# Kernel tuning notes

Hardware: AMD Instinct MI355X
Metric: run time of the kernel (lower is better)

The kernel has to match this reference:

```python
import jax, jax.numpy as jnp
import numpy as np

# dims
B, T1, T2, SEG = 4, 16, 16, 4          # batch, src len, tgt len, max segment length
V, E, H, ENC = 8000, 256, 256, 512     # vocab, embed, lstm hidden, encoder units
EOS = 2                                 # end-of-segment symbol ($)
NEG = -1e30                             # finite -inf (grad-safe)


def setup_inputs():
    key = jax.random.key(0)
    ks = jax.random.split(key, 16)
    s = 0.05
    n = lambda k, shp: (jax.random.normal(k, shp) * s).astype(jnp.float32)
    return {
        "prev_output_tokens": jax.random.randint(ks[0], (B, T2), 0, V),
        "encoder_outs": jax.random.normal(ks[1], (T1, B, ENC), dtype=jnp.float32),
        "embed": n(ks[2], (V, E)),
        "start_embed": n(ks[3], (E,)),
        "proj_h_w": n(ks[4], (H, ENC)), "proj_h_b": jnp.zeros((H,), jnp.float32),
        "proj_c_w": n(ks[5], (H, ENC)), "proj_c_b": jnp.zeros((H,), jnp.float32),
        "w_ih0": n(ks[6], (4 * H, H + E)), "w_hh0": n(ks[7], (4 * H, H)), "b0": jnp.zeros((4 * H,), jnp.float32),
        "w_ih1": n(ks[8], (4 * H, H)), "w_hh1": n(ks[9], (4 * H, H)), "b1": jnp.zeros((4 * H,), jnp.float32),
        "fc_w": n(ks[10], (V, H)), "fc_b": jnp.zeros((V,), jnp.float32),
    }


def _lstm_cell(x, h, c, w_ih, w_hh, b):
    # PyTorch LSTMCell gate order: i, f, g, o
    g = x @ w_ih.T + h @ w_hh.T + b
    i, f, gg, o = jnp.split(g, 4, axis=-1)
    c_new = jax.nn.sigmoid(f) * c + jax.nn.sigmoid(i) * jnp.tanh(gg)
    h_new = jax.nn.sigmoid(o) * jnp.tanh(c_new)
    return h_new, c_new


def reference(prev_output_tokens, encoder_outs, embed, start_embed,
              proj_h_w, proj_h_b, proj_c_w, proj_c_b,
              w_ih0, w_hh0, b0, w_ih1, w_hh1, b1, fc_w, fc_b):
    y = prev_output_tokens                                     # [B, T2]
    # segment windows: tok[b, t2, k] = y[b, t2+k] (clipped; masked later via logpy mask)
    pos = jnp.arange(T2 + 1)[:, None] + jnp.arange(SEG)[None, :]   # [T2+1, SEG]
    tok = y[:, jnp.minimum(pos, T2 - 1)]                            # [B, T2+1, SEG]
    emb_tok = embed[tok]                                            # [B, T2+1, SEG, E]
    x0 = jnp.broadcast_to(start_embed, (B, T2 + 1, 1, E))
    xs = jnp.moveaxis(jnp.concatenate([x0, emb_tok], axis=2), 2, 0)  # [SEG+1, B, T2+1, E]
    tgt = jnp.concatenate([tok, jnp.zeros((B, T2 + 1, 1), tok.dtype)], axis=2)
    tgt = jnp.moveaxis(tgt, 2, 0)                                    # [SEG+1, B, T2+1]

    # per-encoder-position initial states / context (encoder proj, as in __init__)
    eo = jnp.swapaxes(encoder_outs, 0, 1)                            # [B, T1, ENC]
    h0 = eo @ proj_h_w.T + proj_h_b                                  # [B, T1, H]
    c0 = eo @ proj_c_w.T + proj_c_b
    ctx = jnp.broadcast_to(h0[:, :, None, :], (B, T1, T2 + 1, H))

    def step(carry, inp):
        h1, c1, h2, c2 = carry
        x, t = inp                                                   # x [B,T2+1,E], t [B,T2+1]
        xb = jnp.broadcast_to(x[:, None, :, :], (B, T1, T2 + 1, E))
        h1, c1 = _lstm_cell(jnp.concatenate([ctx, xb], axis=-1), h1, c1, w_ih0, w_hh0, b0)
        h2, c2 = _lstm_cell(h1, h2, c2, w_ih1, w_hh1, b1)
        logp = jax.nn.log_softmax(h2 @ fc_w.T + fc_b, axis=-1)       # [B,T1,T2+1,V]
        idx = jnp.broadcast_to(t[:, None, :, None], (B, T1, T2 + 1, 1))
        sel = jnp.take_along_axis(logp, idx, axis=-1)[..., 0]
        return (h1, c1, h2, c2), (sel, logp[..., EOS])

    carry0 = (ctx,
              jnp.broadcast_to(c0[:, :, None, :], (B, T1, T2 + 1, H)),
              jnp.zeros((B, T1, T2 + 1, H), jnp.float32),
              jnp.zeros((B, T1, T2 + 1, H), jnp.float32))
    _, (sel, eosp) = jax.lax.scan(step, carry0, (xs, tgt))           # each [SEG+1,B,T1,T2+1]

    # logpy[b,t1,t2,j] = sum_{k<j} logp_k(y[t2+k]) + logp_j(EOS)
    cum = jnp.concatenate([jnp.zeros((1, B, T1, T2 + 1), sel.dtype),
                           jnp.cumsum(sel[:SEG], axis=0)], axis=0)
    logpy = jnp.moveaxis(cum + eosp, 0, -1)                          # [B,T1,T2+1,SEG+1]
    jmask = (jnp.arange(T2 + 1)[:, None] + jnp.arange(SEG + 1)[None, :]) <= T2
    logpy = jnp.where(jmask[None, None], logpy, NEG)

    # semi-Markov forward DP: alpha[t1+1, t2] = LSE_j alpha[t1, t2-j] + logpy[t1, t2-j, j]
    alpha0 = jnp.full((B, T2 + 1), NEG, sel.dtype).at[:, 0].set(0.0)

    def dp(alpha, row):                                              # row [B, T2+1, SEG+1]
        v = alpha[:, :, None] + row
        shifted = jnp.stack(
            [jnp.pad(v[:, :T2 + 1 - j, j], ((0, 0), (j, 0)), constant_values=NEG)
             for j in range(SEG + 1)], axis=0)
        return jax.nn.logsumexp(shifted, axis=0), None

    alpha, _ = jax.lax.scan(dp, alpha0, jnp.moveaxis(logpy, 1, 0))
    return alpha[:, T2]                                              # log-likelihood per batch elem
```

## Files before the change

kernel.cpp:

```cpp
#include <hip/hip_runtime.h>
#include <math.h>

#define B 4
#define T1 16
#define T2 16
#define SEG 4
#define V 8000
#define E 256
#define H 256
#define ENC 512
#define EOS 2
#define NEGV -1e30f
#define G4 1024
#define NCELL 1088
#define T21 17
#define NL 272
#define MP 5504
#define NTM 43
#define NTN 63
#define NFCT (NTM*NTN)
#define NPART 126

typedef __attribute__((ext_vector_type(4))) float f32x4;
typedef __attribute__((ext_vector_type(8))) short bf16x8;

__device__ __forceinline__ float sigm(float x) { return 1.f / (1.f + __expf(-x)); }
__device__ __forceinline__ float ftanh(float x) { float e = __expf(2.f * x); return 1.f - 2.f / (e + 1.f); }
__device__ __forceinline__ float b2f(short x) {
    unsigned u = ((unsigned)(unsigned short)x) << 16;
    return __builtin_bit_cast(float, u);
}
__device__ __forceinline__ short f2b(float f) {
    unsigned u = __builtin_bit_cast(unsigned, f);
    unsigned r = (u + 0x7fffu + ((u >> 16) & 1u)) >> 16;
    return (short)r;
}

__device__ __forceinline__ int swz8(int row) { return (row & 7) ^ ((row & 3) << 1); }

__device__ __forceinline__ void stage64(const char* g0, size_t gstrideB, int kOffB, char* lds) {
    int tid = threadIdx.x;
#pragma unroll
    for (int it = 0; it < 8; ++it) {
        int chunk = it * 256 + tid;
        int row = chunk >> 5;
        int g = chunk & 31;
        const char* src = g0 + (size_t)row * gstrideB + kOffB + ((g ^ swz8(row)) << 4);
        __builtin_amdgcn_global_load_lds((const __attribute__((address_space(1))) void*)src,
                                         (__attribute__((address_space(3))) void*)(lds + chunk * 16),
                                         16, 0, 0);
    }
}
__device__ __forceinline__ bf16x8 lds_frag(const char* lds, int row, int col16) {
    return *(const bf16x8*)(lds + row * 512 + ((col16 ^ swz8(row)) << 4));
}
__device__ __forceinline__ void mma_tile(const char* smA, const char* smB,
                                         int wave, int ln, int kg, f32x4 acc[4]) {
#pragma unroll
    for (int ks = 0; ks < 8; ++ks) {
        bf16x8 a = lds_frag(smA, wave * 16 + ln, ks * 4 + kg);
#pragma unroll
        for (int nf = 0; nf < 4; ++nf) {
            bf16x8 b = lds_frag(smB, nf * 16 + ln, ks * 4 + kg);
            acc[nf] = __builtin_amdgcn_mfma_f32_16x16x32_bf16(a, b, acc[nf], 0, 0, 0);
        }
    }
}

__device__ __forceinline__ bf16x8 frag128(const char* lds, int row, int gl) {
    return *(const bf16x8*)(lds + row * 256 + ((gl ^ swz8(row)) << 4));
}

__global__ void k_setup(const float* __restrict__ fcw, const float* __restrict__ whh0,
                        const float* __restrict__ wih1, const float* __restrict__ whh1,
                        const float* __restrict__ phw, const float* __restrict__ pcw,
                        const float* __restrict__ wih0, const float* __restrict__ b1,
                        short* __restrict__ fcwbf, short* __restrict__ whh0i, short* __restrict__ w1i,
                        float* __restrict__ projhT, float* __restrict__ projcT,
                        float* __restrict__ ctxT, float* __restrict__ xT, float* __restrict__ b1i) {
    int bid = blockIdx.x, tid = threadIdx.x;
    if (bid < 2000) {
        int i = (bid * 256 + tid) * 4;
        float4 v = *(const float4*)&fcw[i];
        short4 o = { f2b(v.x), f2b(v.y), f2b(v.z), f2b(v.w) };
        *(short4*)&fcwbf[i] = o;
        return;
    }
    bid -= 2000;
    if (bid < 256) {
        int i = (bid * 256 + tid) * 4;
        int gp = i >> 8, k = i & 255;
        float4 v = *(const float4*)&whh0[(size_t)((gp & 3) * 256 + (gp >> 2)) * 256 + k];
        short4 o = { f2b(v.x), f2b(v.y), f2b(v.z), f2b(v.w) };
        *(short4*)&whh0i[i] = o;
        return;
    }
    bid -= 256;
    if (bid < 512) {
        int i = (bid * 256 + tid) * 4;
        int gp = i >> 9, k = i & 511;
        int g = (gp & 3) * 256 + (gp >> 2);
        const float* src = (k < 256) ? &wih1[(size_t)g * 256 + k] : &whh1[(size_t)g * 256 + (k - 256)];
        float4 v = *(const float4*)src;
        short4 o = { f2b(v.x), f2b(v.y), f2b(v.z), f2b(v.w) };
        *(short4*)&w1i[i] = o;
        return;
    }
    bid -= 512;
    if (bid < 128) {
        int i = (bid * 256 + tid) * 4;
        int k = i >> 8, r = i & 255;
        float4 o = { phw[(size_t)r * ENC + k], phw[(size_t)(r + 1) * ENC + k],
                     phw[(size_t)(r + 2) * ENC + k], phw[(size_t)(r + 3) * ENC + k] };
        *(float4*)&projhT[i] = o;
        return;
    }
    bid -= 128;
    if (bid < 128) {
        int i = (bid * 256 + tid) * 4;
        int k = i >> 8, r = i & 255;
        float4 o = { pcw[(size_t)r * ENC + k], pcw[(size_t)(r + 1) * ENC + k],
                     pcw[(size_t)(r + 2) * ENC + k], pcw[(size_t)(r + 3) * ENC + k] };
        *(float4*)&projcT[i] = o;
        return;
    }
    bid -= 128;
    if (bid < 512) {
        int i = (bid * 256 + tid) * 4;
        int g = i >> 9, k = i & 511;
        float4 v = *(const float4*)&wih0[i];
        float* base = (k < 256) ? &ctxT[(size_t)k * G4 + g] : &xT[(size_t)(k - 256) * G4 + g];
        base[0] = v.x; base[G4] = v.y; base[2 * G4] = v.z; base[3 * G4] = v.w;
        return;
    }
    bid -= 512;
    if (bid < 1) {
        float4 o = { b1[tid], b1[256 + tid], b1[512 + tid], b1[768 + tid] };
        *(float4*)&b1i[tid * 4] = o;
        return;
    }
}

__global__ void k_init_state(const float* __restrict__ enc, const float* __restrict__ phT,
                             const float* __restrict__ phb, const float* __restrict__ pcT,
                             const float* __restrict__ pcb, float* __restrict__ h0, float* __restrict__ c0) {
    __shared__ float eo[ENC];
    int bi = blockIdx.x;
    int b = bi / T1, i = bi % T1;
    int j = threadIdx.x;
    for (int e = j; e < ENC; e += 256) eo[e] = enc[(size_t)(i * B + b) * ENC + e];
    __syncthreads();
    float ha = phb[j], ca = pcb[j];
    for (int e = 0; e < ENC; ++e) {
        float x = eo[e];
        ha += x * phT[(size_t)e * H + j];
        ca += x * pcT[(size_t)e * H + j];
    }
    h0[(size_t)bi * H + j] = ha;
    c0[(size_t)bi * H + j] = ca;
}

__global__ void k_init2(const int* __restrict__ y, const float* __restrict__ embed, const float* __restrict__ se,
                        const float* __restrict__ h0, const float* __restrict__ c0,
                        const float* __restrict__ ctxT, const float* __restrict__ xT,
                        const float* __restrict__ b0,
                        float* __restrict__ c1, float* __restrict__ c2,
                        short* __restrict__ hcA, short* __restrict__ hcB,
                        float* __restrict__ pre_ctxi, float* __restrict__ pre_xi) {
    __shared__ float sb[256];
    int bid = blockIdx.x, j = threadIdx.x;
    if (bid < NCELL) {
        int cell = bid, bi = cell / T21;
        c1[(size_t)cell * H + j] = c0[(size_t)bi * H + j];
        c2[(size_t)cell * H + j] = 0.f;
        hcA[(size_t)cell * 512 + j] = f2b(h0[(size_t)bi * H + j]);
        hcB[(size_t)cell * 512 + 256 + j] = 0;
        return;
    }
    bid -= NCELL;
    if (bid < 64) {
        int bi = bid;
        sb[j] = h0[(size_t)bi * H + j];
        __syncthreads();
        float a0 = b0[j], a1 = b0[256 + j], a2 = b0[512 + j], a3 = b0[768 + j];
        for (int k = 0; k < H; ++k) {
            float x = sb[k];
            const float* w = ctxT + (size_t)k * G4;
            a0 += x * w[j]; a1 += x * w[256 + j]; a2 += x * w[512 + j]; a3 += x * w[768 + j];
        }
        *(float4*)&pre_ctxi[(size_t)bi * G4 + 4 * j] = make_float4(a0, a1, a2, a3);
        return;
    }
    bid -= 64;
    int row = bid;
    int s = row / (B * T21), rem = row % (B * T21);
    int b = rem / T21, t = rem % T21;
    const float* src;
    if (s == 0) src = se;
    else { int tt = t + s - 1; if (tt > 15) tt = 15; src = embed + (size_t)y[b * T2 + tt] * E; }
    sb[j] = src[j];
    __syncthreads();
    float a0 = 0, a1 = 0, a2 = 0, a3 = 0;
    for (int k = 0; k < E; ++k) {
        float x = sb[k];
        const float* w = xT + (size_t)k * G4;
        a0 += x * w[j]; a1 += x * w[256 + j]; a2 += x * w[512 + j]; a3 += x * w[768 + j];
    }
    *(float4*)&pre_xi[(size_t)row * G4 + 4 * j] = make_float4(a0, a1, a2, a3);
}

__device__ __forceinline__ void lstm0_body(int step, int l, char* smA, char* smB,
        const short* __restrict__ IN, const short* __restrict__ whh0i,
        const float* __restrict__ pre_ctxi, const float* __restrict__ pre_xi,
        float* __restrict__ c1, short* __restrict__ OUT) {
    int tid = threadIdx.x;
    int wave = tid >> 6, lane = tid & 63, ln = lane & 15, kg = lane >> 4;
    int mb = l >> 4, nb = l & 15;
    int m0 = mb * 64, n0 = nb * 64;
    stage64((const char*)(IN + (size_t)m0 * 512), 1024, 0, smA);
    stage64((const char*)(whh0i + (size_t)n0 * 256), 512, 0, smB);
    __syncthreads();
    f32x4 acc[4] = {};
    mma_tile(smA, smB, wave, ln, kg, acc);
    __syncthreads();
    float* sg = (float*)smA;
#pragma unroll
    for (int nf = 0; nf < 4; ++nf)
#pragma unroll
        for (int r = 0; r < 4; ++r)
            sg[(wave * 16 + kg * 4 + r) * 68 + nf * 16 + ln] = acc[nf][r];
    __syncthreads();
    int jlo = nb * 16;
#pragma unroll
    for (int q2 = 0; q2 < 4; ++q2) {
        int item = q2 * 256 + tid;
        int c = item >> 4, jj = item & 15;
        int cell = m0 + c;
        int j = jlo + jj;
        float4 g = *(float4*)&sg[c * 68 + 4 * jj];
        int bi = cell / T21;
        int bb = bi >> 4;
        int t = cell % T21;
        int prow = (step * B + bb) * T21 + t;
        float4 pc = *(const float4*)&pre_ctxi[(size_t)bi * G4 + 4 * j];
        float4 px = *(const float4*)&pre_xi[(size_t)prow * G4 + 4 * j];
        float ig = g.x + pc.x + px.x, fg = g.y + pc.y + px.y;
        float gg = g.z + pc.z + px.z, og = g.w + pc.w + px.w;
        float cold = c1[(size_t)cell * H + j];
        float cn = sigm(fg) * cold + sigm(ig) * ftanh(gg);
        float hn = sigm(og) * ftanh(cn);
        c1[(size_t)cell * H + j] = cn;
        OUT[(size_t)cell * 512 + j] = f2b(hn);
    }
}

__device__ __forceinline__ void lstm1_body(int l, char* smA, char* smB,
        const short* __restrict__ IN, const short* __restrict__ w1i,
        const float* __restrict__ b1i, float* __restrict__ c2,
        short* __restrict__ slab, short* __restrict__ OUT) {
    int tid = threadIdx.x;
    int wave = tid >> 6, lane = tid & 63, ln = lane & 15, kg = lane >> 4;
    int mb = l >> 4, nb = l & 15;
    int m0 = mb * 64, n0 = nb * 64;
    f32x4 acc[4] = {};
#pragma unroll
    for (int kh = 0; kh < 2; ++kh) {
        if (kh) __syncthreads();
        stage64((const char*)(IN + (size_t)m0 * 512), 1024, kh * 512, smA);
        stage64((const char*)(w1i + (size_t)n0 * 512), 1024, kh * 512, smB);
        __syncthreads();
        mma_tile(smA, smB, wave, ln, kg, acc);
    }
    __syncthreads();
    float* sg = (float*)smA;
#pragma unroll
    for (int nf = 0; nf < 4; ++nf)
#pragma unroll
        for (int r = 0; r < 4; ++r)
            sg[(wave * 16 + kg * 4 + r) * 68 + nf * 16 + ln] = acc[nf][r];
    __syncthreads();
    int jlo = nb * 16;
#pragma unroll
    for (int q2 = 0; q2 < 4; ++q2) {
        int item = q2 * 256 + tid;
        int c = item >> 4, jj = item & 15;
        int cell = m0 + c;
        int j = jlo + jj;
        float4 g = *(float4*)&sg[c * 68 + 4 * jj];
        float4 bv = *(const float4*)&b1i[4 * j];
        float ig = g.x + bv.x, fg = g.y + bv.y, gg = g.z + bv.z, og = g.w + bv.w;
        float cold = c2[(size_t)cell * H + j];
        float cn = sigm(fg) * cold + sigm(ig) * ftanh(gg);
        float hn = sigm(og) * ftanh(cn);
        c2[(size_t)cell * H + j] = cn;
        short hb = f2b(hn);
        slab[(size_t)cell * 256 + j] = hb;
        OUT[(size_t)cell * 512 + 256 + j] = hb;
    }
}

__global__ __launch_bounds__(256, 2) void k_lstm(int s, int n_l1,
        const short* __restrict__ IN, short* __restrict__ OUT, short* __restrict__ slab,
        const short* __restrict__ whh0i, const short* __restrict__ w1i,
        const float* __restrict__ pre_ctxi, const float* __restrict__ pre_xi,
        const float* __restrict__ b1i, float* __restrict__ c1, float* __restrict__ c2) {
    __shared__ char smem[65536];
    char* smA = smem;
    char* smB = smem + 32768;
    int bx = blockIdx.x;
    if (bx < n_l1) lstm1_body(bx, smA, smB, IN, w1i, b1i, c2, slab, OUT);
    else lstm0_body(s + 1, bx - n_l1, smA, smB, IN, whh0i, pre_ctxi, pre_xi, c1, OUT);
}

__global__ __launch_bounds__(256, 2) void k_fc(const short* __restrict__ h2base, const short* __restrict__ Wv,
        const float* __restrict__ fcb, float* __restrict__ psum) {
    __shared__ char smem[65536];
    char* smA = smem;
    char* smB = smem + 32768;
    int bx = blockIdx.x;
    int xcd = bx & 7, idx = bx >> 3;
    int q = NFCT >> 3, r = NFCT & 7;
    int tl = xcd * q + (xcd < r ? xcd : r) + idx;
    int nb = tl / NTM, mb = tl % NTM;
    int m0 = mb * 128, n0 = nb * 128;
    int tid = threadIdx.x;
    int wave = tid >> 6, lane = tid & 63, ln = lane & 15, kg = lane >> 4;
    int wm = wave >> 1, wn = wave & 1;
    f32x4 acc[4][4] = {};
#pragma unroll
    for (int kh = 0; kh < 2; ++kh) {
        if (kh) __syncthreads();
#pragma unroll
        for (int it = 0; it < 8; ++it) {
            int chunk = it * 256 + tid;
            int row = chunk >> 4;
            int g = chunk & 15;
            const char* src = (const char*)(h2base + (size_t)(m0 + row) * 256)
                              + kh * 256 + ((g ^ swz8(row)) << 4);
            __builtin_amdgcn_global_load_lds((const __attribute__((address_space(1))) void*)src,
                                             (__attribute__((address_space(3))) void*)(smA + chunk * 16),
                                             16, 0, 0);
        }
#pragma unroll
        for (int it = 0; it < 8; ++it) {
            int chunk = it * 256 + tid;
            int row = chunk >> 4;
            int g = chunk & 15;
            int grow = n0 + row; if (grow > V - 1) grow = V - 1;
            const char* src = (const char*)(Wv + (size_t)grow * 256)
                              + kh * 256 + ((g ^ swz8(row)) << 4);
            __builtin_amdgcn_global_load_lds((const __attribute__((address_space(1))) void*)src,
                                             (__attribute__((address_space(3))) void*)(smB + chunk * 16),
                                             16, 0, 0);
        }
        __syncthreads();
#pragma unroll
        for (int ks = 0; ks < 4; ++ks) {
            bf16x8 a[4], b[4];
#pragma unroll
            for (int mf = 0; mf < 4; ++mf) a[mf] = frag128(smA, wm * 64 + mf * 16 + ln, ks * 4 + kg);
#pragma unroll
            for (int nf = 0; nf < 4; ++nf) b[nf] = frag128(smB, wn * 64 + nf * 16 + ln, ks * 4 + kg);
#pragma unroll
            for (int mf = 0; mf < 4; ++mf)
#pragma unroll
                for (int nf = 0; nf < 4; ++nf)
                    acc[mf][nf] = __builtin_amdgcn_mfma_f32_16x16x32_bf16(a[mf], b[nf], acc[mf][nf], 0, 0, 0);
        }
    }
    float rs[4][4];
#pragma unroll
    for (int mf = 0; mf < 4; ++mf)
#pragma unroll
        for (int r2 = 0; r2 < 4; ++r2) rs[mf][r2] = 0.f;
#pragma unroll
    for (int nf = 0; nf < 4; ++nf) {
        int col = n0 + wn * 64 + nf * 16 + ln;
        float fbn = (col < V) ? fcb[col] : NEGV;
#pragma unroll
        for (int mf = 0; mf < 4; ++mf)
#pragma unroll
            for (int r2 = 0; r2 < 4; ++r2)
                rs[mf][r2] += __expf(acc[mf][nf][r2] + fbn);
    }
#pragma unroll
    for (int mask = 1; mask < 16; mask <<= 1)
#pragma unroll
        for (int mf = 0; mf < 4; ++mf)
#pragma unroll
            for (int r2 = 0; r2 < 4; ++r2)
                rs[mf][r2] += __shfl_xor(rs[mf][r2], mask);
    if (ln == 0) {
#pragma unroll
        for (int mf = 0; mf < 4; ++mf)
#pragma unroll
            for (int r2 = 0; r2 < 4; ++r2)
                psum[(size_t)(nb * 2 + wn) * MP + m0 + wm * 64 + mf * 16 + kg * 4 + r2] = rs[mf][r2];
    }
}

__global__ void k_combine(const short* __restrict__ h2all, const short* __restrict__ Wv,
        const float* __restrict__ fcb, const int* __restrict__ y,
        const float* __restrict__ psum, float* __restrict__ sel, float* __restrict__ eosp) {
    int cb = blockIdx.x;
    int s = cb / 17, blk = cb % 17;
    int tid = threadIdx.x;
    int cl = tid >> 2, q = tid & 3;
    int cell = blk * 64 + cl;
    int b = cell / (T1 * T21);
    int t = cell % T21;
    int tv = 0;
    if (s < SEG) { int tt = t + s; if (tt > 15) tt = 15; tv = y[b * T2 + tt]; }
    const short* hp = h2all + (size_t)(s + 1) * NCELL * 256 + (size_t)cell * 256 + q * 64;
    const short* w1 = Wv + (size_t)tv * 256 + q * 64;
    const short* w2 = Wv + (size_t)EOS * 256 + q * 64;
    float d1 = 0.f, d2 = 0.f;
#pragma unroll
    for (int u = 0; u < 8; ++u) {
        bf16x8 av  = *(const bf16x8*)(hp + u * 8);
        bf16x8 wv1 = *(const bf16x8*)(w1 + u * 8);
        bf16x8 wv2 = *(const bf16x8*)(w2 + u * 8);
#pragma unroll
        for (int e = 0; e < 8; ++e) {
            float a = b2f(av[e]);
            d1 += a * b2f(wv1[e]);
            d2 += a * b2f(wv2[e]);
        }
    }
    d1 += __shfl_xor(d1, 1); d1 += __shfl_xor(d1, 2);
    d2 += __shfl_xor(d2, 1); d2 += __shfl_xor(d2, 2);
    int col = s * NCELL + cell;
    float ss = 0.f;
    for (int v2 = q * 32; v2 < q * 32 + 32 && v2 < NPART; ++v2)
        ss += psum[(size_t)v2 * MP + col];
    ss += __shfl_xor(ss, 1); ss += __shfl_xor(ss, 2);
    if (q == 0) {
        float lse = __logf(ss);
        sel[s * NCELL + cell]  = d1 + fcb[tv]  - lse;
        eosp[s * NCELL + cell] = d2 + fcb[EOS] - lse;
    }
}

__global__ void k_dp(const float* __restrict__ sel, const float* __restrict__ eosp, float* __restrict__ out) {
    __shared__ float row[SEG + 1][NCELL];
    __shared__ float alpha[B][T21];
    int tid = threadIdx.x;
    for (int c = tid; c < NCELL; c += 256) {
        float cum = 0.f;
        row[0][c] = eosp[c];
#pragma unroll
        for (int j = 1; j <= SEG; ++j) {
            cum += sel[(j - 1) * NCELL + c];
            row[j][c] = cum + eosp[j * NCELL + c];
        }
    }
    int b = tid / T21, t = tid % T21;
    bool act = tid < B * T21;
    if (act) alpha[b][t] = (t == 0) ? 0.f : NEGV;
    __syncthreads();
    for (int i = 0; i < T1; ++i) {
        float val = NEGV;
        if (act) {
            float terms[SEG + 1];
            float mx = -3.4e38f;
            int cnt2 = 0;
            for (int j = 0; j <= SEG && j <= t; ++j) {
                int cell = (b * T1 + i) * T21 + (t - j);
                float term = alpha[b][t - j] + row[j][cell];
                terms[cnt2++] = term;
                mx = fmaxf(mx, term);
            }
            float ssum = 0.f;
            for (int k2 = 0; k2 < cnt2; ++k2) ssum += __expf(terms[k2] - mx);
            val = mx + __logf(ssum);
        }
        __syncthreads();
        if (act) alpha[b][t] = val;
        __syncthreads();
    }
    if (act && t == T2) out[b] = alpha[b][T2];
}

extern "C" void kernel_launch(void* const* d_in, const int* in_sizes, int n_in,
                              void* d_out, int out_size, void* d_ws, size_t ws_size,
                              hipStream_t stream) {
    const int*   y     = (const int*)d_in[0];
    const float* enc   = (const float*)d_in[1];
    const float* embed = (const float*)d_in[2];
    const float* se    = (const float*)d_in[3];
    const float* phw   = (const float*)d_in[4];
    const float* phb   = (const float*)d_in[5];
    const float* pcw   = (const float*)d_in[6];
    const float* pcb   = (const float*)d_in[7];
    const float* wih0  = (const float*)d_in[8];
    const float* whh0  = (const float*)d_in[9];
    const float* b0    = (const float*)d_in[10];
    const float* wih1  = (const float*)d_in[11];
    const float* whh1  = (const float*)d_in[12];
    const float* b1    = (const float*)d_in[13];
    const float* fcw   = (const float*)d_in[14];
    const float* fcb   = (const float*)d_in[15];

    float* ws = (float*)d_ws;
    size_t off = 0;
    auto alloc = [&](size_t n) { float* p = ws + off; off += n; return p; };
    float* projhT   = alloc((size_t)ENC * H);
    float* projcT   = alloc((size_t)ENC * H);
    float* ctxT     = alloc((size_t)H * G4);
    float* xT       = alloc((size_t)E * G4);
    float* h0       = alloc((size_t)B * T1 * H);
    float* c0       = alloc((size_t)B * T1 * H);
    float* pre_ctxi = alloc((size_t)B * T1 * G4);
    float* pre_xi   = alloc((size_t)(SEG + 1) * B * T21 * G4);
    float* c1       = alloc((size_t)NCELL * H);
    float* c2       = alloc((size_t)NCELL * H);
    float* b1i      = alloc((size_t)G4);
    float* selbuf   = alloc((size_t)(SEG + 1) * NCELL);
    float* eospbuf  = alloc((size_t)(SEG + 1) * NCELL);
    float* psum     = alloc((size_t)NPART * MP);
    short* hc0      = (short*)alloc((size_t)NCELL * 512 / 2);
    short* hc1      = (short*)alloc((size_t)NCELL * 512 / 2);
    short* h2all    = (short*)alloc(((size_t)6 * NCELL + 64) * 256 / 2);
    short* whh0i    = (short*)alloc((size_t)G4 * 256 / 2);
    short* w1i      = (short*)alloc((size_t)G4 * 512 / 2);
    short* fcwbf    = (short*)alloc((size_t)V * H / 2);

    hipLaunchKernelGGL(k_setup, dim3(3537), dim3(256), 0, stream,
                       fcw, whh0, wih1, whh1, phw, pcw, wih0, b1,
                       fcwbf, whh0i, w1i, projhT, projcT, ctxT, xT, b1i);
    hipLaunchKernelGGL(k_init_state, dim3(B * T1), dim3(256), 0, stream,
                       enc, projhT, phb, projcT, pcb, h0, c0);
    hipLaunchKernelGGL(k_init2, dim3(NCELL + 64 + (SEG + 1) * B * T21), dim3(256), 0, stream,
                       y, embed, se, h0, c0, ctxT, xT, b0, c1, c2, hc0, hc1,
                       pre_ctxi, pre_xi);

    short* hcb[2] = { hc0, hc1 };
    hipLaunchKernelGGL(k_lstm, dim3(NL), dim3(256), 0, stream,
                       -1, 0, hcb[0], hcb[1], h2all,
                       whh0i, w1i, pre_ctxi, pre_xi, b1i, c1, c2);
    for (int s = 0; s < SEG; ++s) {
        hipLaunchKernelGGL(k_lstm, dim3(2 * NL), dim3(256), 0, stream,
                           s, NL, hcb[(s + 1) & 1], hcb[s & 1],
                           h2all + (size_t)(s + 1) * NCELL * 256,
                           whh0i, w1i, pre_ctxi, pre_xi, b1i, c1, c2);
    }
    hipLaunchKernelGGL(k_lstm, dim3(NL), dim3(256), 0, stream,
                       4, NL, hcb[1], hcb[0],
                       h2all + (size_t)5 * NCELL * 256,
                       whh0i, w1i, pre_ctxi, pre_xi, b1i, c1, c2);

    hipLaunchKernelGGL(k_fc, dim3(NFCT), dim3(256), 0, stream,
                       h2all + (size_t)NCELL * 256, fcwbf, fcb, psum);
    hipLaunchKernelGGL(k_combine, dim3(85), dim3(256), 0, stream,
                       h2all, fcwbf, fcb, y, psum, selbuf, eospbuf);
    hipLaunchKernelGGL(k_dp, dim3(1), dim3(256), 0, stream, selbuf, eospbuf, (float*)d_out);
}
```

Baseline: 186.6 us.

## Fuse all phases into one cooperative persistent kernel with grid syncs

Replaces the chain of roughly a dozen separate kernel launches (setup, init, per-step LSTM, FC, combine, DP) with a single cooperative kernel of 256 blocks that runs each phase in grid-stride loops separated by grid-wide barriers. This removes per-launch overhead and the gaps between dependent launches. In exchange each phase is limited to a fixed grid of 256 blocks with a 128KB LDS footprint, which lowers occupancy for the wide phases such as the FC GEMM and setup. Grid syncs also cost time. If the cooperative launch fails, it falls back to per-phase launches.

```diff
diff --git a/kernel.cpp b/kernel.cpp
--- a/kernel.cpp
+++ b/kernel.cpp
@@ -1,5 +1,8 @@
 #include <hip/hip_runtime.h>
+#include <hip/hip_cooperative_groups.h>
 #include <math.h>
+
+namespace cg = cooperative_groups;
 
 #define B 4
 #define T1 16
@@ -14,15 +17,25 @@
 #define G4 1024
 #define NCELL 1088
 #define T21 17
-#define NL 272
 #define MP 5504
 #define NTM 43
-#define NTN 63
-#define NFCT (NTM*NTN)
 #define NPART 126
+#define GRID 256
 
 typedef __attribute__((ext_vector_type(4))) float f32x4;
 typedef __attribute__((ext_vector_type(8))) short bf16x8;
+
+struct P {
+    const int* y; const float* enc; const float* embed; const float* se;
+    const float* phw; const float* phb; const float* pcw; const float* pcb;
+    const float* wih0; const float* whh0; const float* b0;
+    const float* wih1; const float* whh1; const float* b1;
+    const float* fcw; const float* fcb;
+    float *projhT, *projcT, *ctxT, *xT, *h0, *c0, *pre_ctxi, *pre_xi, *c1, *c2, *b1i;
+    float *selbuf, *eospbuf, *psum;
+    short *hc0, *hc1, *h2all, *whh0i, *w1i, *fcwbf;
+    float* out;
+};
 
 __device__ __forceinline__ float sigm(float x) { return 1.f / (1.f + __expf(-x)); }
 __device__ __forceinline__ float ftanh(float x) { float e = __expf(2.f * x); return 1.f - 2.f / (e + 1.f); }
@@ -35,7 +48,6 @@
     unsigned r = (u + 0x7fffu + ((u >> 16) & 1u)) >> 16;
     return (short)r;
 }
-
 __device__ __forceinline__ int swz8(int row) { return (row & 7) ^ ((row & 3) << 1); }
 
 __device__ __forceinline__ void stage64(const char* g0, size_t gstrideB, int kOffB, char* lds) {
@@ -66,164 +78,145 @@
         }
     }
 }
-
 __device__ __forceinline__ bf16x8 frag128(const char* lds, int row, int gl) {
     return *(const bf16x8*)(lds + row * 256 + ((gl ^ swz8(row)) << 4));
 }
 
-__global__ void k_setup(const float* __restrict__ fcw, const float* __restrict__ whh0,
-                        const float* __restrict__ wih1, const float* __restrict__ whh1,
-                        const float* __restrict__ phw, const float* __restrict__ pcw,
-                        const float* __restrict__ wih0, const float* __restrict__ b1,
-                        short* __restrict__ fcwbf, short* __restrict__ whh0i, short* __restrict__ w1i,
-                        float* __restrict__ projhT, float* __restrict__ projcT,
-                        float* __restrict__ ctxT, float* __restrict__ xT, float* __restrict__ b1i) {
-    int bid = blockIdx.x, tid = threadIdx.x;
-    if (bid < 2000) {
-        int i = (bid * 256 + tid) * 4;
-        float4 v = *(const float4*)&fcw[i];
-        short4 o = { f2b(v.x), f2b(v.y), f2b(v.z), f2b(v.w) };
-        *(short4*)&fcwbf[i] = o;
-        return;
-    }
-    bid -= 2000;
-    if (bid < 256) {
-        int i = (bid * 256 + tid) * 4;
-        int gp = i >> 8, k = i & 255;
-        float4 v = *(const float4*)&whh0[(size_t)((gp & 3) * 256 + (gp >> 2)) * 256 + k];
-        short4 o = { f2b(v.x), f2b(v.y), f2b(v.z), f2b(v.w) };
-        *(short4*)&whh0i[i] = o;
-        return;
-    }
-    bid -= 256;
-    if (bid < 512) {
-        int i = (bid * 256 + tid) * 4;
-        int gp = i >> 9, k = i & 511;
-        int g = (gp & 3) * 256 + (gp >> 2);
-        const float* src = (k < 256) ? &wih1[(size_t)g * 256 + k] : &whh1[(size_t)g * 256 + (k - 256)];
-        float4 v = *(const float4*)src;
-        short4 o = { f2b(v.x), f2b(v.y), f2b(v.z), f2b(v.w) };
-        *(short4*)&w1i[i] = o;
-        return;
-    }
-    bid -= 512;
-    if (bid < 128) {
-        int i = (bid * 256 + tid) * 4;
-        int k = i >> 8, r = i & 255;
-        float4 o = { phw[(size_t)r * ENC + k], phw[(size_t)(r + 1) * ENC + k],
-                     phw[(size_t)(r + 2) * ENC + k], phw[(size_t)(r + 3) * ENC + k] };
-        *(float4*)&projhT[i] = o;
-        return;
-    }
-    bid -= 128;
-    if (bid < 128) {
-        int i = (bid * 256 + tid) * 4;
-        int k = i >> 8, r = i & 255;
-        float4 o = { pcw[(size_t)r * ENC + k], pcw[(size_t)(r + 1) * ENC + k],
-                     pcw[(size_t)(r + 2) * ENC + k], pcw[(size_t)(r + 3) * ENC + k] };
-        *(float4*)&projcT[i] = o;
-        return;
-    }
-    bid -= 128;
-    if (bid < 512) {
-        int i = (bid * 256 + tid) * 4;
-        int g = i >> 9, k = i & 511;
-        float4 v = *(const float4*)&wih0[i];
-        float* base = (k < 256) ? &ctxT[(size_t)k * G4 + g] : &xT[(size_t)(k - 256) * G4 + g];
-        base[0] = v.x; base[G4] = v.y; base[2 * G4] = v.z; base[3 * G4] = v.w;
-        return;
-    }
-    bid -= 512;
-    if (bid < 1) {
-        float4 o = { b1[tid], b1[256 + tid], b1[512 + tid], b1[768 + tid] };
-        *(float4*)&b1i[tid * 4] = o;
-        return;
-    }
-}
-
-__global__ void k_init_state(const float* __restrict__ enc, const float* __restrict__ phT,
-                             const float* __restrict__ phb, const float* __restrict__ pcT,
-                             const float* __restrict__ pcb, float* __restrict__ h0, float* __restrict__ c0) {
-    __shared__ float eo[ENC];
+
+__device__ void phase_setup(const P& p) {
+    int tid = threadIdx.x;
+    for (int u = blockIdx.x; u < 3537; u += gridDim.x) {
+        int bid = u;
+        if (bid < 2000) {
+            int i = (bid * 256 + tid) * 4;
+            float4 v = *(const float4*)&p.fcw[i];
+            short4 o = { f2b(v.x), f2b(v.y), f2b(v.z), f2b(v.w) };
+            *(short4*)&p.fcwbf[i] = o;
+            continue;
+        }
+        bid -= 2000;
+        if (bid < 256) {
+            int i = (bid * 256 + tid) * 4;
+            int gp = i >> 8, k = i & 255;
+            float4 v = *(const float4*)&p.whh0[(size_t)((gp & 3) * 256 + (gp >> 2)) * 256 + k];
+            short4 o = { f2b(v.x), f2b(v.y), f2b(v.z), f2b(v.w) };
+            *(short4*)&p.whh0i[i] = o;
+            continue;
+        }
+        bid -= 256;
+        if (bid < 512) {
+            int i = (bid * 256 + tid) * 4;
+            int gp = i >> 9, k = i & 511;
+            int g = (gp & 3) * 256 + (gp >> 2);
+            const float* src = (k < 256) ? &p.wih1[(size_t)g * 256 + k] : &p.whh1[(size_t)g * 256 + (k - 256)];
+            float4 v = *(const float4*)src;
+            short4 o = { f2b(v.x), f2b(v.y), f2b(v.z), f2b(v.w) };
+            *(short4*)&p.w1i[i] = o;
+            continue;
+        }
+        bid -= 512;
+        if (bid < 128) {
+            int i = (bid * 256 + tid) * 4;
+            int k = i >> 8, r = i & 255;
+            float4 o = { p.phw[(size_t)r * ENC + k], p.phw[(size_t)(r + 1) * ENC + k],
+                         p.phw[(size_t)(r + 2) * ENC + k], p.phw[(size_t)(r + 3) * ENC + k] };
+            *(float4*)&p.projhT[i] = o;
+            continue;
+        }
+        bid -= 128;
+        if (bid < 128) {
+            int i = (bid * 256 + tid) * 4;
+            int k = i >> 8, r = i & 255;
+            float4 o = { p.pcw[(size_t)r * ENC + k], p.pcw[(size_t)(r + 1) * ENC + k],
+                         p.pcw[(size_t)(r + 2) * ENC + k], p.pcw[(size_t)(r + 3) * ENC + k] };
+            *(float4*)&p.projcT[i] = o;
+            continue;
+        }
+        bid -= 128;
+        if (bid < 512) {
+            int i = (bid * 256 + tid) * 4;
+            int g = i >> 9, k = i & 511;
+            float4 v = *(const float4*)&p.wih0[i];
+            float* base = (k < 256) ? &p.ctxT[(size_t)k * G4 + g] : &p.xT[(size_t)(k - 256) * G4 + g];
+            base[0] = v.x; base[G4] = v.y; base[2 * G4] = v.z; base[3 * G4] = v.w;
+            continue;
+        }
+        bid -= 512;
+        if (bid < 1) {
+            float4 o = { p.b1[tid], p.b1[256 + tid], p.b1[512 + tid], p.b1[768 + tid] };
+            *(float4*)&p.b1i[tid * 4] = o;
+        }
+    }
+}
+
+__device__ void phase_init_state(const P& p, char* smem) {
     int bi = blockIdx.x;
+    if (bi >= 64) return;
+    float* eo = (float*)smem;
     int b = bi / T1, i = bi % T1;
     int j = threadIdx.x;
-    for (int e = j; e < ENC; e += 256) eo[e] = enc[(size_t)(i * B + b) * ENC + e];
-    __syncthreads();
-    float ha = phb[j], ca = pcb[j];
+    for (int e = j; e < ENC; e += 256) eo[e] = p.enc[(size_t)(i * B + b) * ENC + e];
+    __syncthreads();
+    float ha = p.phb[j], ca = p.pcb[j];
     for (int e = 0; e < ENC; ++e) {
         float x = eo[e];
-        ha += x * phT[(size_t)e * H + j];
-        ca += x * pcT[(size_t)e * H + j];
-    }
-    h0[(size_t)bi * H + j] = ha;
-    c0[(size_t)bi * H + j] = ca;
-}
-
-__global__ void k_init2(const int* __restrict__ y, const float* __restrict__ embed, const float* __restrict__ se,
-                        const float* __restrict__ h0, const float* __restrict__ c0,
-                        const float* __restrict__ ctxT, const float* __restrict__ xT,
-                        const float* __restrict__ b0,
-                        float* __restrict__ c1, float* __restrict__ c2,
-                        short* __restrict__ hcA, short* __restrict__ hcB,
-                        float* __restrict__ pre_ctxi, float* __restrict__ pre_xi) {
-    __shared__ float sb[256];
-    int bid = blockIdx.x, j = threadIdx.x;
-    if (bid < NCELL) {
-        int cell = bid, bi = cell / T21;
-        c1[(size_t)cell * H + j] = c0[(size_t)bi * H + j];
-        c2[(size_t)cell * H + j] = 0.f;
-        hcA[(size_t)cell * 512 + j] = f2b(h0[(size_t)bi * H + j]);
-        hcB[(size_t)cell * 512 + 256 + j] = 0;
-        return;
-    }
-    bid -= NCELL;
-    if (bid < 64) {
-        int bi = bid;
-        sb[j] = h0[(size_t)bi * H + j];
-        __syncthreads();
-        float a0 = b0[j], a1 = b0[256 + j], a2 = b0[512 + j], a3 = b0[768 + j];
-        for (int k = 0; k < H; ++k) {
+        ha += x * p.projhT[(size_t)e * H + j];
+        ca += x * p.projcT[(size_t)e * H + j];
+    }
+    p.h0[(size_t)bi * H + j] = ha;
+    p.c0[(size_t)bi * H + j] = ca;
+}
+
+__device__ void phase_init2(const P& p, char* smem) {
+    float* sb = (float*)smem;
+    int j = threadIdx.x;
+    for (int u = blockIdx.x; u < NCELL + 64 + (SEG + 1) * B * T21; u += gridDim.x) {
+        int bid = u;
+        if (bid < NCELL) {
+            int cell = bid, bi = cell / T21;
+            p.c1[(size_t)cell * H + j] = p.c0[(size_t)bi * H + j];
+            p.c2[(size_t)cell * H + j] = 0.f;
+            p.hc0[(size_t)cell * 512 + j] = f2b(p.h0[(size_t)bi * H + j]);
+            p.hc1[(size_t)cell * 512 + 256 + j] = 0;
+            continue;
+        }
+        bid -= NCELL;
+        if (bid < 64) {
+            int bi = bid;
+            __syncthreads();
+            sb[j] = p.h0[(size_t)bi * H + j];
+            __syncthreads();
+            float a0 = p.b0[j], a1 = p.b0[256 + j], a2 = p.b0[512 + j], a3 = p.b0[768 + j];
+            for (int k = 0; k < H; ++k) {
+                float x = sb[k];
+                const float* w = p.ctxT + (size_t)k * G4;
+                a0 += x * w[j]; a1 += x * w[256 + j]; a2 += x * w[512 + j]; a3 += x * w[768 + j];
+            }
+            *(float4*)&p.pre_ctxi[(size_t)bi * G4 + 4 * j] = make_float4(a0, a1, a2, a3);
+            continue;
+        }
+        bid -= 64;
+        int row = bid;
+        int s = row / (B * T21), rem = row % (B * T21);
+        int b = rem / T21, t = rem % T21;
+        const float* src;
+        if (s == 0) src = p.se;
+        else { int tt = t + s - 1; if (tt > 15) tt = 15; src = p.embed + (size_t)p.y[b * T2 + tt] * E; }
+        __syncthreads();
+        sb[j] = src[j];
+        __syncthreads();
+        float a0 = 0, a1 = 0, a2 = 0, a3 = 0;
+        for (int k = 0; k < E; ++k) {
             float x = sb[k];
-            const float* w = ctxT + (size_t)k * G4;
+            const float* w = p.xT + (size_t)k * G4;
             a0 += x * w[j]; a1 += x * w[256 + j]; a2 += x * w[512 + j]; a3 += x * w[768 + j];
         }
-        *(float4*)&pre_ctxi[(size_t)bi * G4 + 4 * j] = make_float4(a0, a1, a2, a3);
-        return;
-    }
-    bid -= 64;
-    int row = bid;
-    int s = row / (B * T21), rem = row % (B * T21);
-    int b = rem / T21, t = rem % T21;
-    const float* src;
-    if (s == 0) src = se;
-    else { int tt = t + s - 1; if (tt > 15) tt = 15; src = embed + (size_t)y[b * T2 + tt] * E; }
-    sb[j] = src[j];
-    __syncthreads();
-    float a0 = 0, a1 = 0, a2 = 0, a3 = 0;
-    for (int k = 0; k < E; ++k) {
-        float x = sb[k];
-        const float* w = xT + (size_t)k * G4;
-        a0 += x * w[j]; a1 += x * w[256 + j]; a2 += x * w[512 + j]; a3 += x * w[768 + j];
-    }
-    *(float4*)&pre_xi[(size_t)row * G4 + 4 * j] = make_float4(a0, a1, a2, a3);
-}
-
-__device__ __forceinline__ void lstm0_body(int step, int l, char* smA, char* smB,
-        const short* __restrict__ IN, const short* __restrict__ whh0i,
-        const float* __restrict__ pre_ctxi, const float* __restrict__ pre_xi,
-        float* __restrict__ c1, short* __restrict__ OUT) {
-    int tid = threadIdx.x;
-    int wave = tid >> 6, lane = tid & 63, ln = lane & 15, kg = lane >> 4;
-    int mb = l >> 4, nb = l & 15;
-    int m0 = mb * 64, n0 = nb * 64;
-    stage64((const char*)(IN + (size_t)m0 * 512), 1024, 0, smA);
-    stage64((const char*)(whh0i + (size_t)n0 * 256), 512, 0, smB);
-    __syncthreads();
-    f32x4 acc[4] = {};
-    mma_tile(smA, smB, wave, ln, kg, acc);
-    __syncthreads();
-    float* sg = (float*)smA;
+        *(float4*)&p.pre_xi[(size_t)row * G4 + 4 * j] = make_float4(a0, a1, a2, a3);
+    }
+}
+
+__device__ void epi_l0(const P& p, float* sg, f32x4 acc[4], int m0, int nb, int step, short* OUT) {
+    int tid = threadIdx.x, wave = tid >> 6, lane = tid & 63, ln = lane & 15, kg = lane >> 4;
 #pragma unroll
     for (int nf = 0; nf < 4; ++nf)
 #pragma unroll
@@ -242,43 +235,28 @@
         int bb = bi >> 4;
         int t = cell % T21;
         int prow = (step * B + bb) * T21 + t;
-        float4 pc = *(const float4*)&pre_ctxi[(size_t)bi * G4 + 4 * j];
-        float4 px = *(const float4*)&pre_xi[(size_t)prow * G4 + 4 * j];
+        float4 pc = *(const float4*)&p.pre_ctxi[(size_t)bi * G4 + 4 * j];
+        float4 px = *(const float4*)&p.pre_xi[(size_t)prow * G4 + 4 * j];
         float ig = g.x + pc.x + px.x, fg = g.y + pc.y + px.y;
         float gg = g.z + pc.z + px.z, og = g.w + pc.w + px.w;
-        float cold = c1[(size_t)cell * H + j];
+        float cold = p.c1[(size_t)cell * H + j];
         float cn = sigm(fg) * cold + sigm(ig) * ftanh(gg);
         float hn = sigm(og) * ftanh(cn);
-        c1[(size_t)cell * H + j] = cn;
+        p.c1[(size_t)cell * H + j] = cn;
         OUT[(size_t)cell * 512 + j] = f2b(hn);
     }
-}
-
-__device__ __forceinline__ void lstm1_body(int l, char* smA, char* smB,
-        const short* __restrict__ IN, const short* __restrict__ w1i,
-        const float* __restrict__ b1i, float* __restrict__ c2,
-        short* __restrict__ slab, short* __restrict__ OUT) {
-    int tid = threadIdx.x;
-    int wave = tid >> 6, lane = tid & 63, ln = lane & 15, kg = lane >> 4;
-    int mb = l >> 4, nb = l & 15;
-    int m0 = mb * 64, n0 = nb * 64;
-    f32x4 acc[4] = {};
-#pragma unroll
-    for (int kh = 0; kh < 2; ++kh) {
-        if (kh) __syncthreads();
-        stage64((const char*)(IN + (size_t)m0 * 512), 1024, kh * 512, smA);
-        stage64((const char*)(w1i + (size_t)n0 * 512), 1024, kh * 512, smB);
-        __syncthreads();
-        mma_tile(smA, smB, wave, ln, kg, acc);
-    }
-    __syncthreads();
-    float* sg = (float*)smA;
+    __syncthreads();
+}
+
+__device__ void epi_l1(const P& p, float* sg, f32x4 acc[4], int m0, int nb, int s, short* OUT, bool writeOUT) {
+    int tid = threadIdx.x, wave = tid >> 6, lane = tid & 63, ln = lane & 15, kg = lane >> 4;
 #pragma unroll
     for (int nf = 0; nf < 4; ++nf)
 #pragma unroll
         for (int r = 0; r < 4; ++r)
             sg[(wave * 16 + kg * 4 + r) * 68 + nf * 16 + ln] = acc[nf][r];
     __syncthreads();
+    short* slab = p.h2all + (size_t)(s + 1) * NCELL * 256;
     int jlo = nb * 16;
 #pragma unroll
     for (int q2 = 0; q2 < 4; ++q2) {
@@ -287,122 +265,181 @@
         int cell = m0 + c;
         int j = jlo + jj;
         float4 g = *(float4*)&sg[c * 68 + 4 * jj];
-        float4 bv = *(const float4*)&b1i[4 * j];
+        float4 bv = *(const float4*)&p.b1i[4 * j];
         float ig = g.x + bv.x, fg = g.y + bv.y, gg = g.z + bv.z, og = g.w + bv.w;
-        float cold = c2[(size_t)cell * H + j];
+        float cold = p.c2[(size_t)cell * H + j];
         float cn = sigm(fg) * cold + sigm(ig) * ftanh(gg);
         float hn = sigm(og) * ftanh(cn);
-        c2[(size_t)cell * H + j] = cn;
+        p.c2[(size_t)cell * H + j] = cn;
         short hb = f2b(hn);
         slab[(size_t)cell * 256 + j] = hb;
-        OUT[(size_t)cell * 512 + 256 + j] = hb;
-    }
-}
-
-__global__ __launch_bounds__(256, 2) void k_lstm(int s, int n_l1,
-        const short* __restrict__ IN, short* __restrict__ OUT, short* __restrict__ slab,
-        const short* __restrict__ whh0i, const short* __restrict__ w1i,
-        const float* __restrict__ pre_ctxi, const float* __restrict__ pre_xi,
-        const float* __restrict__ b1i, float* __restrict__ c1, float* __restrict__ c2) {
-    __shared__ char smem[65536];
-    char* smA = smem;
-    char* smB = smem + 32768;
-    int bx = blockIdx.x;
-    if (bx < n_l1) lstm1_body(bx, smA, smB, IN, w1i, b1i, c2, slab, OUT);
-    else lstm0_body(s + 1, bx - n_l1, smA, smB, IN, whh0i, pre_ctxi, pre_xi, c1, OUT);
-}
-
-__global__ __launch_bounds__(256, 2) void k_fc(const short* __restrict__ h2base, const short* __restrict__ Wv,
-        const float* __restrict__ fcb, float* __restrict__ psum) {
-    __shared__ char smem[65536];
-    char* smA = smem;
-    char* smB = smem + 32768;
-    int bx = blockIdx.x;
-    int xcd = bx & 7, idx = bx >> 3;
-    int q = NFCT >> 3, r = NFCT & 7;
-    int tl = xcd * q + (xcd < r ? xcd : r) + idx;
-    int nb = tl / NTM, mb = tl % NTM;
-    int m0 = mb * 128, n0 = nb * 128;
-    int tid = threadIdx.x;
+        if (writeOUT) OUT[(size_t)cell * 512 + 256 + j] = hb;
+    }
+    __syncthreads();
+}
+
+__device__ void phase_lstm(const P& p, char* smem, int s1, int s0, bool doB) {
+    int bx = blockIdx.x, tid = threadIdx.x;
     int wave = tid >> 6, lane = tid & 63, ln = lane & 15, kg = lane >> 4;
-    int wm = wave >> 1, wn = wave & 1;
-    f32x4 acc[4][4] = {};
+    int nb = bx & 15, mb = bx >> 4;
+    char* A  = smem;
+    char* B0 = smem + 32768;
+    char* B1 = smem + 65536;
+    char* B2 = smem + 98304;
+    if (doB) {
+        stage64((const char*)(p.whh0i + (size_t)nb * 64 * 256), 512, 0, B0);
+        stage64((const char*)(p.w1i + (size_t)nb * 64 * 512), 1024, 0, B1);
+        stage64((const char*)(p.w1i + (size_t)nb * 64 * 512), 1024, 512, B2);
+    }
+    int sin = (s0 >= 0) ? s0 - 1 : s1;
+    const short* IN = ((sin + 1) & 1) ? p.hc1 : p.hc0;
+    short* OUT = (sin & 1) ? p.hc1 : p.hc0;
+    f32x4 acc1[4] = {}, acc0[4] = {};
+    stage64((const char*)(IN + (size_t)mb * 64 * 512), 1024, 0, A);
+    __syncthreads();
+    if (s1 >= 0) mma_tile(A, B1, wave, ln, kg, acc1);
+    if (s0 >= 0) mma_tile(A, B0, wave, ln, kg, acc0);
+    __syncthreads();
+    if (s1 >= 0) {
+        stage64((const char*)(IN + (size_t)mb * 64 * 512), 1024, 512, A);
+        __syncthreads();
+        mma_tile(A, B2, wave, ln, kg, acc1);
+        __syncthreads();
+        epi_l1(p, (float*)A, acc1, mb * 64, nb, s1, OUT, s1 != SEG);
+    }
+    if (s0 >= 0)
+        epi_l0(p, (float*)A, acc0, mb * 64, nb, s0, OUT);
+    if (s1 >= 0 && mb == 15) {
+        f32x4 e1[4] = {};
+        stage64((const char*)(IN + (size_t)1024 * 512), 1024, 0, A);
+        __syncthreads();
+        mma_tile(A, B1, wave, ln, kg, e1);
+        __syncthreads();
+        stage64((const char*)(IN + (size_t)1024 * 512), 1024, 512, A);
+        __syncthreads();
+        mma_tile(A, B2, wave, ln, kg, e1);
+        __syncthreads();
+        epi_l1(p, (float*)A, e1, 1024, nb, s1, OUT, s1 != SEG);
+    }
+    if (s0 >= 0 && mb == 14) {
+        f32x4 e0[4] = {};
+        stage64((const char*)(IN + (size_t)1024 * 512), 1024, 0, A);
+        __syncthreads();
+        mma_tile(A, B0, wave, ln, kg, e0);
+        __syncthreads();
+        epi_l0(p, (float*)A, e0, 1024, nb, s0, OUT);
+    }
+}
+
+__device__ void phase_fc(const P& p, char* smem) {
+    int bx = blockIdx.x, tid = threadIdx.x;
+    char* Ab0 = smem;
+    char* Ab1 = smem + 32768;
+    char* Bh0 = smem + 65536;
+    char* Bh1 = smem + 98304;
+    int t6 = bx & 63, w2 = bx >> 6;
+    int nb, w;
+    if (t6 == 63) { nb = w2; w = 4; } else { nb = t6; w = w2; }
+    int nw = (nb < 4) ? 5 : 4;
+    int n0 = nb * 128;
 #pragma unroll
     for (int kh = 0; kh < 2; ++kh) {
-        if (kh) __syncthreads();
-#pragma unroll
-        for (int it = 0; it < 8; ++it) {
-            int chunk = it * 256 + tid;
-            int row = chunk >> 4;
-            int g = chunk & 15;
-            const char* src = (const char*)(h2base + (size_t)(m0 + row) * 256)
-                              + kh * 256 + ((g ^ swz8(row)) << 4);
-            __builtin_amdgcn_global_load_lds((const __attribute__((address_space(1))) void*)src,
-                                             (__attribute__((address_space(3))) void*)(smA + chunk * 16),
-                                             16, 0, 0);
-        }
+        char* dst = kh ? Bh1 : Bh0;
 #pragma unroll
         for (int it = 0; it < 8; ++it) {
             int chunk = it * 256 + tid;
             int row = chunk >> 4;
             int g = chunk & 15;
             int grow = n0 + row; if (grow > V - 1) grow = V - 1;
-            const char* src = (const char*)(Wv + (size_t)grow * 256)
-                              + kh * 256 + ((g ^ swz8(row)) << 4);
+            const char* src = (const char*)(p.fcwbf + (size_t)grow * 256) + kh * 256 + ((g ^ swz8(row)) << 4);
             __builtin_amdgcn_global_load_lds((const __attribute__((address_space(1))) void*)src,
-                                             (__attribute__((address_space(3))) void*)(smB + chunk * 16),
+                                             (__attribute__((address_space(3))) void*)(dst + chunk * 16),
                                              16, 0, 0);
         }
-        __syncthreads();
+    }
+    int mbs[11]; int cnt = 0;
+    for (int mb = w; mb < NTM; mb += nw) mbs[cnt++] = mb;
+    const short* h2base = p.h2all + (size_t)NCELL * 256;
+    auto stageA = [&](int mb, int kh, char* buf) {
+#pragma unroll
+        for (int it = 0; it < 8; ++it) {
+            int chunk = it * 256 + tid;
+            int row = chunk >> 4;
+            int g = chunk & 15;
+            const char* src = (const char*)(h2base + (size_t)(mb * 128 + row) * 256) + kh * 256 + ((g ^ swz8(row)) << 4);
+            __builtin_amdgcn_global_load_lds((const __attribute__((address_space(1))) void*)src,
+                                             (__attribute__((address_space(3))) void*)(buf + chunk * 16),
+                                             16, 0, 0);
+        }
+    };
+    stageA(mbs[0], 0, Ab0);
+    __syncthreads();
+    int wave = tid >> 6, lane = tid & 63, ln = lane & 15, kg = lane >> 4;
+    int wm = wave >> 1, wn = wave & 1;
+    f32x4 acc[4][4] = {};
+    int nst = cnt * 2;
+    for (int st = 0; st < nst; ++st) {
+        int mb = mbs[st >> 1], kh = st & 1;
+        if (st + 1 < nst) stageA(mbs[(st + 1) >> 1], (st + 1) & 1, ((st + 1) & 1) ? Ab1 : Ab0);
+        char* Acur = (st & 1) ? Ab1 : Ab0;
+        char* Bcur = kh ? Bh1 : Bh0;
 #pragma unroll
         for (int ks = 0; ks < 4; ++ks) {
             bf16x8 a[4], b[4];
 #pragma unroll
-            for (int mf = 0; mf < 4; ++mf) a[mf] = frag128(smA, wm * 64 + mf * 16 + ln, ks * 4 + kg);
-#pragma unroll
-            for (int nf = 0; nf < 4; ++nf) b[nf] = frag128(smB, wn * 64 + nf * 16 + ln, ks * 4 + kg);
+            for (int mf = 0; mf < 4; ++mf) a[mf] = frag128(Acur, wm * 64 + mf * 16 + ln, ks * 4 + kg);
+#pragma unroll
+            for (int nf = 0; nf < 4; ++nf) b[nf] = frag128(Bcur, wn * 64 + nf * 16 + ln, ks * 4 + kg);
 #pragma unroll
             for (int mf = 0; mf < 4; ++mf)
 #pragma unroll
                 for (int nf = 0; nf < 4; ++nf)
                     acc[mf][nf] = __builtin_amdgcn_mfma_f32_16x16x32_bf16(a[mf], b[nf], acc[mf][nf], 0, 0, 0);
         }
-    }
-    float rs[4][4];
-#pragma unroll
-    for (int mf = 0; mf < 4; ++mf)
-#pragma unroll
-        for (int r2 = 0; r2 < 4; ++r2) rs[mf][r2] = 0.f;
-#pragma unroll
-    for (int nf = 0; nf < 4; ++nf) {
-        int col = n0 + wn * 64 + nf * 16 + ln;
-        float fbn = (col < V) ? fcb[col] : NEGV;
-#pragma unroll
-        for (int mf = 0; mf < 4; ++mf)
-#pragma unroll
-            for (int r2 = 0; r2 < 4; ++r2)
-                rs[mf][r2] += __expf(acc[mf][nf][r2] + fbn);
-    }
-#pragma unroll
-    for (int mask = 1; mask < 16; mask <<= 1)
-#pragma unroll
-        for (int mf = 0; mf < 4; ++mf)
-#pragma unroll
-            for (int r2 = 0; r2 < 4; ++r2)
-                rs[mf][r2] += __shfl_xor(rs[mf][r2], mask);
-    if (ln == 0) {
-#pragma unroll
-        for (int mf = 0; mf < 4; ++mf)
-#pragma unroll
-            for (int r2 = 0; r2 < 4; ++r2)
-                psum[(size_t)(nb * 2 + wn) * MP + m0 + wm * 64 + mf * 16 + kg * 4 + r2] = rs[mf][r2];
-    }
-}
-
-__global__ void k_combine(const short* __restrict__ h2all, const short* __restrict__ Wv,
-        const float* __restrict__ fcb, const int* __restrict__ y,
-        const float* __restrict__ psum, float* __restrict__ sel, float* __restrict__ eosp) {
+        if (kh) {
+            int m0 = mb * 128;
+            float rs[4][4];
+#pragma unroll
+            for (int mf = 0; mf < 4; ++mf)
+#pragma unroll
+                for (int r2 = 0; r2 < 4; ++r2) rs[mf][r2] = 0.f;
+#pragma unroll
+            for (int nf = 0; nf < 4; ++nf) {
+                int col = n0 + wn * 64 + nf * 16 + ln;
+                float fbn = (col < V) ? p.fcb[col] : NEGV;
+#pragma unroll
+                for (int mf = 0; mf < 4; ++mf)
+#pragma unroll
+                    for (int r2 = 0; r2 < 4; ++r2)
+                        rs[mf][r2] += __expf(acc[mf][nf][r2] + fbn);
+            }
+#pragma unroll
+            for (int mask = 1; mask < 16; mask <<= 1)
+#pragma unroll
+                for (int mf = 0; mf < 4; ++mf)
+#pragma unroll
+                    for (int r2 = 0; r2 < 4; ++r2)
+                        rs[mf][r2] += __shfl_xor(rs[mf][r2], mask);
+            if (ln == 0) {
+#pragma unroll
+                for (int mf = 0; mf < 4; ++mf)
+#pragma unroll
+                    for (int r2 = 0; r2 < 4; ++r2)
+                        p.psum[(size_t)(nb * 2 + wn) * MP + m0 + wm * 64 + mf * 16 + kg * 4 + r2] = rs[mf][r2];
+            }
+#pragma unroll
+            for (int mf = 0; mf < 4; ++mf)
+#pragma unroll
+                for (int nf = 0; nf < 4; ++nf)
+                    acc[mf][nf] = f32x4{0.f, 0.f, 0.f, 0.f};
+        }
+        __syncthreads();
+    }
+}
+
+__device__ void phase_combine(const P& p) {
     int cb = blockIdx.x;
+    if (cb >= 85) return;
     int s = cb / 17, blk = cb % 17;
     int tid = threadIdx.x;
     int cl = tid >> 2, q = tid & 3;
@@ -410,10 +447,10 @@
     int b = cell / (T1 * T21);
     int t = cell % T21;
     int tv = 0;
-    if (s < SEG) { int tt = t + s; if (tt > 15) tt = 15; tv = y[b * T2 + tt]; }
-    const short* hp = h2all + (size_t)(s + 1) * NCELL * 256 + (size_t)cell * 256 + q * 64;
-    const short* w1 = Wv + (size_t)tv * 256 + q * 64;
-    const short* w2 = Wv + (size_t)EOS * 256 + q * 64;
+    if (s < SEG) { int tt = t + s; if (tt > 15) tt = 15; tv = p.y[b * T2 + tt]; }
+    const short* hp = p.h2all + (size_t)(s + 1) * NCELL * 256 + (size_t)cell * 256 + q * 64;
+    const short* w1 = p.fcwbf + (size_t)tv * 256 + q * 64;
+    const short* w2 = p.fcwbf + (size_t)EOS * 256 + q * 64;
     float d1 = 0.f, d2 = 0.f;
 #pragma unroll
     for (int u = 0; u < 8; ++u) {
@@ -432,31 +469,32 @@
     int col = s * NCELL + cell;
     float ss = 0.f;
     for (int v2 = q * 32; v2 < q * 32 + 32 && v2 < NPART; ++v2)
-        ss += psum[(size_t)v2 * MP + col];
+        ss += p.psum[(size_t)v2 * MP + col];
     ss += __shfl_xor(ss, 1); ss += __shfl_xor(ss, 2);
     if (q == 0) {
         float lse = __logf(ss);
-        sel[s * NCELL + cell]  = d1 + fcb[tv]  - lse;
-        eosp[s * NCELL + cell] = d2 + fcb[EOS] - lse;
-    }
-}
-
-__global__ void k_dp(const float* __restrict__ sel, const float* __restrict__ eosp, float* __restrict__ out) {
-    __shared__ float row[SEG + 1][NCELL];
-    __shared__ float alpha[B][T21];
+        p.selbuf[s * NCELL + cell]  = d1 + p.fcb[tv]  - lse;
+        p.eospbuf[s * NCELL + cell] = d2 + p.fcb[EOS] - lse;
+    }
+}
+
+__device__ void phase_dp(const P& p, char* smem) {
+    if (blockIdx.x != 0) return;
+    float* row = (float*)smem;
+    float* alpha = (float*)(smem + (SEG + 1) * NCELL * 4);
     int tid = threadIdx.x;
     for (int c = tid; c < NCELL; c += 256) {
         float cum = 0.f;
-        row[0][c] = eosp[c];
+        row[c] = p.eospbuf[c];
 #pragma unroll
         for (int j = 1; j <= SEG; ++j) {
-            cum += sel[(j - 1) * NCELL + c];
-            row[j][c] = cum + eosp[j * NCELL + c];
+            cum += p.selbuf[(j - 1) * NCELL + c];
+            row[j * NCELL + c] = cum + p.eospbuf[j * NCELL + c];
         }
     }
     int b = tid / T21, t = tid % T21;
     bool act = tid < B * T21;
-    if (act) alpha[b][t] = (t == 0) ? 0.f : NEGV;
+    if (act) alpha[b * T21 + t] = (t == 0) ? 0.f : NEGV;
     __syncthreads();
     for (int i = 0; i < T1; ++i) {
         float val = NEGV;
@@ -466,7 +504,7 @@
             int cnt2 = 0;
             for (int j = 0; j <= SEG && j <= t; ++j) {
                 int cell = (b * T1 + i) * T21 + (t - j);
-                float term = alpha[b][t - j] + row[j][cell];
+                float term = alpha[b * T21 + t - j] + row[j * NCELL + cell];
                 terms[cnt2++] = term;
                 mx = fmaxf(mx, term);
             }
@@ -475,83 +513,98 @@
             val = mx + __logf(ssum);
         }
         __syncthreads();
-        if (act) alpha[b][t] = val;
-        __syncthreads();
-    }
-    if (act && t == T2) out[b] = alpha[b][T2];
+        if (act) alpha[b * T21 + t] = val;
+        __syncthreads();
+    }
+    if (act && t == T2) p.out[b] = alpha[b * T21 + T2];
+}
+
+__global__ void k_mega(P p) {
+    __shared__ __align__(16) char smem[131072];
+    cg::grid_group g = cg::this_grid();
+    phase_setup(p);                       g.sync();
+    phase_init_state(p, smem);            g.sync();
+    phase_init2(p, smem);                 g.sync();
+    phase_lstm(p, smem, -1, 0, true);     g.sync();
+    phase_lstm(p, smem, 0, 1, false);     g.sync();
+    phase_lstm(p, smem, 1, 2, false);     g.sync();
+    phase_lstm(p, smem, 2, 3, false);     g.sync();
+    phase_lstm(p, smem, 3, 4, false);     g.sync();
+    phase_lstm(p, smem, 4, -1, false);    g.sync();
+    phase_fc(p, smem);                    g.sync();
+    phase_combine(p);                     g.sync();
+    phase_dp(p, smem);
+}
+
+__global__ void kw_phase(P p, int ph) {
+    __shared__ __align__(16) char smem[131072];
+    switch (ph) {
+        case 0:  phase_setup(p); break;
+        case 1:  phase_init_state(p, smem); break;
+        case 2:  phase_init2(p, smem); break;
+        case 3:  phase_lstm(p, smem, -1, 0, true); break;
+        case 4:  phase_lstm(p, smem, 0, 1, true); break;
+        case 5:  phase_lstm(p, smem, 1, 2, true); break;
+        case 6:  phase_lstm(p, smem, 2, 3, true); break;
+        case 7:  phase_lstm(p, smem, 3, 4, true); break;
+        case 8:  phase_lstm(p, smem, 4, -1, true); break;
+        case 9:  phase_fc(p, smem); break;
+        case 10: phase_combine(p); break;
+        case 11: phase_dp(p, smem); break;
+    }
 }
 
 extern "C" void kernel_launch(void* const* d_in, const int* in_sizes, int n_in,
                               void* d_out, int out_size, void* d_ws, size_t ws_size,
                               hipStream_t stream) {
-    const int*   y     = (const int*)d_in[0];
-    const float* enc   = (const float*)d_in[1];
-    const float* embed = (const float*)d_in[2];
-    const float* se    = (const float*)d_in[3];
-    const float* phw   = (const float*)d_in[4];
-    const float* phb   = (const float*)d_in[5];
-    const float* pcw   = (const float*)d_in[6];
-    const float* pcb   = (const float*)d_in[7];
-    const float* wih0  = (const float*)d_in[8];
-    const float* whh0  = (const float*)d_in[9];
-    const float* b0    = (const float*)d_in[10];
-    const float* wih1  = (const float*)d_in[11];
-    const float* whh1  = (const float*)d_in[12];
-    const float* b1    = (const float*)d_in[13];
-    const float* fcw   = (const float*)d_in[14];
-    const float* fcb   = (const float*)d_in[15];
+    P prm;
+    prm.y     = (const int*)d_in[0];
+    prm.enc   = (const float*)d_in[1];
+    prm.embed = (const float*)d_in[2];
+    prm.se    = (const float*)d_in[3];
+    prm.phw   = (const float*)d_in[4];
+    prm.phb   = (const float*)d_in[5];
+    prm.pcw   = (const float*)d_in[6];
+    prm.pcb   = (const float*)d_in[7];
+    prm.wih0  = (const float*)d_in[8];
+    prm.whh0  = (const float*)d_in[9];
+    prm.b0    = (const float*)d_in[10];
+    prm.wih1  = (const float*)d_in[11];
+    prm.whh1  = (const float*)d_in[12];
+    prm.b1    = (const float*)d_in[13];
+    prm.fcw   = (const float*)d_in[14];
+    prm.fcb   = (const float*)d_in[15];
 
     float* ws = (float*)d_ws;
     size_t off = 0;
-    auto alloc = [&](size_t n) { float* p = ws + off; off += n; return p; };
-    float* projhT   = alloc((size_t)ENC * H);
-    float* projcT   = alloc((size_t)ENC * H);
-    float* ctxT     = alloc((size_t)H * G4);
-    float* xT       = alloc((size_t)E * G4);
-    float* h0       = alloc((size_t)B * T1 * H);
-    float* c0       = alloc((size_t)B * T1 * H);
-    float* pre_ctxi = alloc((size_t)B * T1 * G4);
-    float* pre_xi   = alloc((size_t)(SEG + 1) * B * T21 * G4);
-    float* c1       = alloc((size_t)NCELL * H);
-    float* c2       = alloc((size_t)NCELL * H);
-    float* b1i      = alloc((size_t)G4);
-    float* selbuf   = alloc((size_t)(SEG + 1) * NCELL);
-    float* eospbuf  = alloc((size_t)(SEG + 1) * NCELL);
-    float* psum     = alloc((size_t)NPART * MP);
-    short* hc0      = (short*)alloc((size_t)NCELL * 512 / 2);
-    short* hc1      = (short*)alloc((size_t)NCELL * 512 / 2);
-    short* h2all    = (short*)alloc(((size_t)6 * NCELL + 64) * 256 / 2);
-    short* whh0i    = (short*)alloc((size_t)G4 * 256 / 2);
-    short* w1i      = (short*)alloc((size_t)G4 * 512 / 2);
-    short* fcwbf    = (short*)alloc((size_t)V * H / 2);
-
-    hipLaunchKernelGGL(k_setup, dim3(3537), dim3(256), 0, stream,
-                       fcw, whh0, wih1, whh1, phw, pcw, wih0, b1,
-                       fcwbf, whh0i, w1i, projhT, projcT, ctxT, xT, b1i);
-    hipLaunchKernelGGL(k_init_state, dim3(B * T1), dim3(256), 0, stream,
-                       enc, projhT, phb, projcT, pcb, h0, c0);
-    hipLaunchKernelGGL(k_init2, dim3(NCELL + 64 + (SEG + 1) * B * T21), dim3(256), 0, stream,
-                       y, embed, se, h0, c0, ctxT, xT, b0, c1, c2, hc0, hc1,
-                       pre_ctxi, pre_xi);
-
-    short* hcb[2] = { hc0, hc1 };
-    hipLaunchKernelGGL(k_lstm, dim3(NL), dim3(256), 0, stream,
-                       -1, 0, hcb[0], hcb[1], h2all,
-                       whh0i, w1i, pre_ctxi, pre_xi, b1i, c1, c2);
-    for (int s = 0; s < SEG; ++s) {
-        hipLaunchKernelGGL(k_lstm, dim3(2 * NL), dim3(256), 0, stream,
-                           s, NL, hcb[(s + 1) & 1], hcb[s & 1],
-                           h2all + (size_t)(s + 1) * NCELL * 256,
-                           whh0i, w1i, pre_ctxi, pre_xi, b1i, c1, c2);
-    }
-    hipLaunchKernelGGL(k_lstm, dim3(NL), dim3(256), 0, stream,
-                       4, NL, hcb[1], hcb[0],
-                       h2all + (size_t)5 * NCELL * 256,
-                       whh0i, w1i, pre_ctxi, pre_xi, b1i, c1, c2);
-
-    hipLaunchKernelGGL(k_fc, dim3(NFCT), dim3(256), 0, stream,
-                       h2all + (size_t)NCELL * 256, fcwbf, fcb, psum);
-    hipLaunchKernelGGL(k_combine, dim3(85), dim3(256), 0, stream,
-                       h2all, fcwbf, fcb, y, psum, selbuf, eospbuf);
-    hipLaunchKernelGGL(k_dp, dim3(1), dim3(256), 0, stream, selbuf, eospbuf, (float*)d_out);
-}
+    auto alloc = [&](size_t n) { float* pp = ws + off; off += n; return pp; };
+    prm.projhT   = alloc((size_t)ENC * H);
+    prm.projcT   = alloc((size_t)ENC * H);
+    prm.ctxT     = alloc((size_t)H * G4);
+    prm.xT       = alloc((size_t)E * G4);
+    prm.h0       = alloc((size_t)B * T1 * H);
+    prm.c0       = alloc((size_t)B * T1 * H);
+    prm.pre_ctxi = alloc((size_t)B * T1 * G4);
+    prm.pre_xi   = alloc((size_t)(SEG + 1) * B * T21 * G4);
+    prm.c1       = alloc((size_t)NCELL * H);
+    prm.c2       = alloc((size_t)NCELL * H);
+    prm.b1i      = alloc((size_t)G4);
+    prm.selbuf   = alloc((size_t)(SEG + 1) * NCELL);
+    prm.eospbuf  = alloc((size_t)(SEG + 1) * NCELL);
+    prm.psum     = alloc((size_t)NPART * MP);
+    prm.hc0      = (short*)alloc((size_t)NCELL * 512 / 2);
+    prm.hc1      = (short*)alloc((size_t)NCELL * 512 / 2);
+    prm.h2all    = (short*)alloc(((size_t)6 * NCELL + 64) * 256 / 2);
+    prm.whh0i    = (short*)alloc((size_t)G4 * 256 / 2);
+    prm.w1i      = (short*)alloc((size_t)G4 * 512 / 2);
+    prm.fcwbf    = (short*)alloc((size_t)V * H / 2);
+    prm.out      = (float*)d_out;
+
+    void* args[] = { (void*)&prm };
+    hipError_t err = hipLaunchCooperativeKernel((const void*)k_mega, dim3(GRID), dim3(256),
+                                                args, 0, stream);
+    if (err != hipSuccess) {
+        for (int ph = 0; ph < 12; ++ph)
+            hipLaunchKernelGGL(kw_phase, dim3(GRID), dim3(256), 0, stream, prm, ph);
+    }
+}
```

Result: slower. 655.8 us (+251.4%).
